# Optimization experiments

Measured on AMD Instinct MI355X. Metric: run time of the kernel, lower is better.

The kernel has to match this reference:

```python
import jax, jax.numpy as jnp
import numpy as np

B, S, D, H, DH = 2, 4096, 768, 12, 64
L = 2                      # encoder layers (reduced-depth longformer-base)
HW = 256                   # one-sided sliding window (attention_window = 512)
C = 2 * HW                 # query chunk size
NC = S // C                # number of chunks
KW = C + 2 * HW            # key-window length per chunk
V = 50265
SEP_ID, NSEP = 2, 32       # </s> token id; SEPs per block (fixed by construction)
G = NSEP + 1               # global tokens: <s> at pos 0 + all SEPs
NCLS = 5
EPS = 1e-5
NEG = -1e9


def layer_norm(x, gb):
    m = jnp.mean(x, -1, keepdims=True)
    v = jnp.var(x, -1, keepdims=True)
    return (x - m) * jax.lax.rsqrt(v + EPS) * gb[0] + gb[1]


def split_heads(x):  # [B,S,D] -> [B,H,S,DH]
    return x.reshape(B, S, H, DH).transpose(0, 2, 1, 3)


def window_gather(x):  # [B,H,S,DH] -> [B,H,NC,KW,DH] overlapping key windows
    xp = jnp.pad(x, ((0, 0), (0, 0), (HW, HW), (0, 0)))
    idx = (jnp.arange(NC) * C)[:, None] + jnp.arange(KW)[None, :]
    return xp[:, :, idx, :]


def longformer_attn(x, amask, gpos, wqkv, bqkv, wqkv_g, bqkv_g, wo, bo):
    q = split_heads(x @ wqkv[0] + bqkv[0]) / np.float32(np.sqrt(DH))
    k = split_heads(x @ wqkv[1] + bqkv[1])
    v = split_heads(x @ wqkv[2] + bqkv[2])

    # ----- local sliding-window scores (banded, chunked) -----
    kw = window_gather(k)
    vw = window_gather(v)
    qc = q.reshape(B, H, NC, C, DH)
    s_loc = jnp.einsum('bhncd,bhnkd->bhnck', qc, kw)  # [B,H,NC,C,KW]

    rel = jnp.arange(KW)[None, :] - jnp.arange(C)[:, None]          # [C,KW]
    band_ok = (rel >= 0) & (rel <= 2 * HW)
    key_pos = (jnp.arange(NC) * C)[:, None] + jnp.arange(KW)[None, :] - HW
    in_b = (key_pos >= 0) & (key_pos < S)                            # [NC,KW]
    amp = jnp.pad(amask, ((0, 0), (HW, HW)))
    idx = (jnp.arange(NC) * C)[:, None] + jnp.arange(KW)[None, :]
    am_w = amp[:, idx] > 0                                           # [B,NC,KW]
    mask = band_ok[None, None, None] & in_b[None, None, :, None, :] & am_w[:, None, :, None, :]
    s_loc = jnp.where(mask, s_loc, NEG).reshape(B, H, S, KW)

    # ----- scores of every query against the G global keys -----
    gidx = gpos[:, None, :, None]                                    # [B,1,G,1]
    kg = jnp.take_along_axis(k, gidx, axis=2)                        # [B,H,G,DH]
    vg = jnp.take_along_axis(v, gidx, axis=2)
    s_glob = jnp.einsum('bhsd,bhgd->bhsg', q, kg)                    # [B,H,S,G]

    probs = jax.nn.softmax(jnp.concatenate([s_glob, s_loc], -1), -1)
    pg, pl = probs[..., :G], probs[..., G:]
    ctx = jnp.einsum('bhsg,bhgd->bhsd', pg, vg)
    ctx = ctx + jnp.einsum('bhnck,bhnkd->bhncd', pl.reshape(B, H, NC, C, KW), vw).reshape(B, H, S, DH)

    # ----- global tokens attend to everything (separate projections) -----
    qg = split_heads(x @ wqkv_g[0] + bqkv_g[0]) / np.float32(np.sqrt(DH))
    kgf = split_heads(x @ wqkv_g[1] + bqkv_g[1])
    vgf = split_heads(x @ wqkv_g[2] + bqkv_g[2])
    qg = jnp.take_along_axis(qg, gidx, axis=2)                       # [B,H,G,DH]
    s_g = jnp.einsum('bhgd,bhsd->bhgs', qg, kgf)                     # [B,H,G,S]
    s_g = jnp.where(amask[:, None, None, :] > 0, s_g, NEG)
    og = jnp.einsum('bhgs,bhsd->bhgd', jax.nn.softmax(s_g, -1), vgf)

    ctx_m = ctx.transpose(0, 2, 1, 3).reshape(B, S, D)
    og_m = og.transpose(0, 2, 1, 3).reshape(B, G, D)
    ctx_m = ctx_m.at[jnp.arange(B)[:, None], gpos].set(og_m)         # replace global rows
    return ctx_m @ wo + bo


def setup_inputs() -> dict:
    key = jax.random.key(0)
    ks = jax.random.split(key, 12)
    ids = jax.random.randint(ks[0], (B, S), 5, V, dtype=jnp.int32)
    sep_positions = (jnp.arange(NSEP) + 1) * (S // NSEP) - 1         # SEP every 128 toks
    ids = ids.at[:, sep_positions].set(SEP_ID).at[:, 0].set(0)       # <s> at pos 0
    att = jnp.ones((B, S), jnp.int32)

    def nrm(k, shp):
        return jax.random.normal(k, shp, jnp.float32) * 0.02

    ln = jnp.stack([jnp.ones(D, jnp.float32), jnp.zeros(D, jnp.float32)])
    return dict(
        input_ids=ids, attention_mask=att,
        word_emb=nrm(ks[1], (V, D)), pos_emb=nrm(ks[2], (S + 2, D)),
        type_emb=nrm(ks[3], (D,)), emb_ln=ln,
        Wqkv=nrm(ks[4], (L, 3, D, D)), bqkv=jnp.zeros((L, 3, D), jnp.float32),
        Wqkv_g=nrm(ks[5], (L, 3, D, D)), bqkv_g=jnp.zeros((L, 3, D), jnp.float32),
        Wo=nrm(ks[6], (L, D, D)), bo=jnp.zeros((L, D), jnp.float32),
        ln1=jnp.broadcast_to(ln, (L, 2, D)),
        Wff1=nrm(ks[7], (L, D, 4 * D)), bff1=jnp.zeros((L, 4 * D), jnp.float32),
        Wff2=nrm(ks[8], (L, 4 * D, D)), bff2=jnp.zeros((L, D), jnp.float32),
        ln2=jnp.broadcast_to(ln, (L, 2, D)),
        cls_W=nrm(ks[9], (NCLS, D)), cls_b=jnp.zeros((NCLS,), jnp.float32),
    )


def reference(input_ids, attention_mask, word_emb, pos_emb, type_emb, emb_ln,
              Wqkv, bqkv, Wqkv_g, bqkv_g, Wo, bo, ln1, Wff1, bff1, Wff2, bff2,
              ln2, cls_W, cls_b):
    # global attention mask: pos 0 + every SEP (fixed count by construction)
    sep_pos = jnp.sort(jnp.where(input_ids == SEP_ID, jnp.arange(S)[None, :], S), -1)[:, :NSEP]
    sep_pos = sep_pos.astype(jnp.int32)
    gpos = jnp.concatenate([jnp.zeros((B, 1), jnp.int32), sep_pos], 1)  # [B,G]

    x = word_emb[input_ids] + pos_emb[jnp.arange(S) + 2][None] + type_emb
    x = layer_norm(x, emb_ln)
    for l in range(L):
        a = longformer_attn(x, attention_mask, gpos, Wqkv[l], bqkv[l],
                            Wqkv_g[l], bqkv_g[l], Wo[l], bo[l])
        x = layer_norm(x + a, ln1[l])
        f = jax.nn.gelu(x @ Wff1[l] + bff1[l], approximate=False) @ Wff2[l] + bff2[l]
        x = layer_norm(x + f, ln2[l])

    # gather SEP embeddings (row-major over batch then sentence) -> classifier
    h = jnp.take_along_axis(x, sep_pos[:, :, None], axis=1).reshape(B * NSEP, D)
    return h @ cls_W.T + cls_b
```

## Files before the change

### kernel.cpp

```cpp
#include <hip/hip_runtime.h>


#define Bb 2
#define Ss 4096
#define Dd 768
#define Hh 12
#define Gg 33
#define NSEPn 32
#define Ll 2
#define SPAD 4640
#define PADL 256
#define NCLSn 5
#define NCH 16
#define PARTF 1056
#define PSTR 72

typedef unsigned short u16;
typedef __attribute__((ext_vector_type(8))) short bv8;
typedef __attribute__((ext_vector_type(4))) short sv4;
typedef __attribute__((ext_vector_type(4))) float f32x4;

__device__ __forceinline__ float bf2f(u16 u) {
  unsigned v = ((unsigned)u) << 16;
  return __builtin_bit_cast(float, v);
}
__device__ __forceinline__ u16 f2bf(float f) {
  unsigned u = __builtin_bit_cast(unsigned, f);
  u += 0x7fffu + ((u >> 16) & 1u);
  return (u16)(u >> 16);
}
__device__ __forceinline__ void glds16(const void* g, void* l) {
  __builtin_amdgcn_global_load_lds(
      (const __attribute__((address_space(1))) void*)g,
      (__attribute__((address_space(3))) void*)l, 16, 0, 0);
}

__global__ void sep_find_kernel(const int* __restrict__ ids, int* __restrict__ cnt,
                                int* __restrict__ list) {
  int i = blockIdx.x * 256 + threadIdx.x;
  if (i >= Bb * Ss) return;
  int b = i >> 12;
  if (ids[i] == 2) {
    int idx = atomicAdd(&cnt[b], 1);
    if (idx < 64) list[b * 64 + idx] = i & (Ss - 1);
  }
}

__global__ void sep_sort_kernel(const int* __restrict__ cnt, const int* __restrict__ list,
                                int* __restrict__ gpos) {
  int b = blockIdx.x;
  int t = threadIdx.x;
  int n = cnt[b]; if (n > 64) n = 64;
  if (t < Gg) gpos[b * Gg + t] = (t == 0) ? 0 : (Ss - 1);
  __syncthreads();
  if (t < n) {
    int v = list[b * 64 + t];
    int rank = 0;
    for (int j = 0; j < n; ++j) rank += (list[b * 64 + j] < v) ? 1 : 0;
    if (rank < NSEPn) gpos[b * Gg + 1 + rank] = v;
  }
}

__global__ __launch_bounds__(256)
void wconv_kernel(const float* __restrict__ src0, u16* __restrict__ dst0,
                  int K, int N, int grp, long unit, long WLs) {
  __shared__ float t[32][33];
  int z = blockIdx.z;
  const float* src = src0 + (size_t)z * K * N;
  u16* dst = dst0 + (size_t)(z / grp) * WLs + (size_t)(z % grp) * unit;
  int n0 = blockIdx.x * 32, k0 = blockIdx.y * 32;
  int tx = threadIdx.x & 31, ty = threadIdx.x >> 5;
  #pragma unroll
  for (int i = 0; i < 4; ++i)
    t[ty + i * 8][tx] = src[(size_t)(k0 + ty + i * 8) * N + n0 + tx];
  __syncthreads();
  #pragma unroll
  for (int i = 0; i < 4; ++i)
    dst[(size_t)(n0 + ty + i * 8) * K + k0 + tx] = f2bf(t[tx][ty + i * 8]);
}

__global__ __launch_bounds__(256)
void embed_ln_kernel(const int* __restrict__ ids, const float* __restrict__ we,
                     const float* __restrict__ pe, const float* __restrict__ te,
                     const float* __restrict__ lnp, float* __restrict__ x,
                     u16* __restrict__ xb) {
  int row = blockIdx.x;
  int s = row & (Ss - 1);
  int id = ids[row];
  int tid = threadIdx.x;
  float v[3]; float sm = 0.f, s2 = 0.f;
  #pragma unroll
  for (int i = 0; i < 3; ++i) {
    int c = tid + i * 256;
    float t = we[(size_t)id * Dd + c] + pe[(size_t)(s + 2) * Dd + c] + te[c];
    v[i] = t; sm += t; s2 += t * t;
  }
  __shared__ float r1[256], r2[256];
  r1[tid] = sm; r2[tid] = s2; __syncthreads();
  for (int o = 128; o; o >>= 1) {
    if (tid < o) { r1[tid] += r1[tid + o]; r2[tid] += r2[tid + o]; }
    __syncthreads();
  }
  float mean = r1[0] * (1.f / 768.f);
  float var  = r2[0] * (1.f / 768.f) - mean * mean;
  float rs = rsqrtf(var + 1e-5f);
  #pragma unroll
  for (int i = 0; i < 3; ++i) {
    int c = tid + i * 256;
    float o = (v[i] - mean) * rs * lnp[c] + lnp[Dd + c];
    x[(size_t)row * Dd + c] = o;
    xb[(size_t)row * Dd + c] = f2bf(o);
  }
}

__global__ __launch_bounds__(256)
void add_ln3_kernel(const float* __restrict__ xin, const float* __restrict__ y0,
                    const float* __restrict__ y1, const float* __restrict__ lnp,
                    float* __restrict__ xout, u16* __restrict__ xbout) {
  int row = blockIdx.x;
  int tid = threadIdx.x;
  float v[3]; float sm = 0.f, s2 = 0.f;
  #pragma unroll
  for (int i = 0; i < 3; ++i) {
    int c = tid + i * 256;
    size_t idx = (size_t)row * Dd + c;
    float t = xin[idx] + y0[idx] + y1[idx];
    v[i] = t; sm += t; s2 += t * t;
  }
  __shared__ float r1[256], r2[256];
  r1[tid] = sm; r2[tid] = s2; __syncthreads();
  for (int o = 128; o; o >>= 1) {
    if (tid < o) { r1[tid] += r1[tid + o]; r2[tid] += r2[tid + o]; }
    __syncthreads();
  }
  float mean = r1[0] * (1.f / 768.f);
  float var  = r2[0] * (1.f / 768.f) - mean * mean;
  float rs = rsqrtf(var + 1e-5f);
  #pragma unroll
  for (int i = 0; i < 3; ++i) {
    int c = tid + i * 256;
    float o = (v[i] - mean) * rs * lnp[c] + lnp[Dd + c];
    xout[(size_t)row * Dd + c] = o;
    xbout[(size_t)row * Dd + c] = f2bf(o);
  }
}

template <int MODE>
__global__ __launch_bounds__(256)
void gemm2_kernel(const u16* __restrict__ A, const u16* __restrict__ Bt,
                  const float* __restrict__ bias, float* __restrict__ outf,
                  float* __restrict__ outf2,
                  u16* __restrict__ o0, u16* __restrict__ o1, u16* __restrict__ o2,
                  int N, int Ks, int Kl, float scale) {
  __shared__ u16 la[2][128 * 32], lb[2][128 * 32];
  int tid = threadIdx.x;
  int wave = tid >> 6, lane = tid & 63;
  int wr = wave >> 1, wc = wave & 1;
  int lg = lane >> 4, lc = lane & 15;
  int row0 = blockIdx.y * 128, col0 = blockIdx.x * 128;
  int koff = blockIdx.z * Kl;

  const u16* Ag = A + (size_t)(row0 + wave * 32 + (lane >> 2)) * Ks + (lane & 3) * 8 + koff;
  const u16* Bg = Bt + (size_t)(col0 + wave * 32 + (lane >> 2)) * Ks + (lane & 3) * 8 + koff;
  int wofs = wave * 1024;

  f32x4 acc[4][4];
  #pragma unroll
  for (int m = 0; m < 4; ++m)
    #pragma unroll
    for (int n = 0; n < 4; ++n) acc[m][n] = (f32x4){0.f, 0.f, 0.f, 0.f};

  glds16(Ag, la[0] + wofs);
  glds16(Ag + (size_t)16 * Ks, la[0] + wofs + 512);
  glds16(Bg, lb[0] + wofs);
  glds16(Bg + (size_t)16 * Ks, lb[0] + wofs + 512);
  __syncthreads();

  int nk = Kl >> 5;
  for (int t = 0; t < nk; ++t) {
    int cur = t & 1;
    if (t + 1 < nk) {
      int k1 = (t + 1) << 5;
      glds16(Ag + k1, la[cur ^ 1] + wofs);
      glds16(Ag + (size_t)16 * Ks + k1, la[cur ^ 1] + wofs + 512);
      glds16(Bg + k1, lb[cur ^ 1] + wofs);
      glds16(Bg + (size_t)16 * Ks + k1, lb[cur ^ 1] + wofs + 512);
    }
    bv8 af[4], bf_[4];
    #pragma unroll
    for (int m = 0; m < 4; ++m)
      af[m] = *reinterpret_cast<const bv8*>(la[cur] + (wr * 64 + m * 16 + lc) * 32 + lg * 8);
    #pragma unroll
    for (int n = 0; n < 4; ++n)
      bf_[n] = *reinterpret_cast<const bv8*>(lb[cur] + (wc * 64 + n * 16 + lc) * 32 + lg * 8);
    __builtin_amdgcn_s_setprio(1);
    #pragma unroll
    for (int m = 0; m < 4; ++m)
      #pragma unroll
      for (int n = 0; n < 4; ++n)
        acc[m][n] = __builtin_amdgcn_mfma_f32_16x16x32_bf16(af[m], bf_[n], acc[m][n], 0, 0, 0);
    __builtin_amdgcn_s_setprio(0);
    __syncthreads();
  }

  #pragma unroll
  for (int m = 0; m < 4; ++m) {
    int grow0 = row0 + wr * 64 + m * 16 + lg * 4;
    #pragma unroll
    for (int n = 0; n < 4; ++n) {
      int gcol = col0 + wc * 64 + n * 16 + lc;
      float bvl = bias[gcol];
      if (MODE == 0) {
        float* od = blockIdx.z ? outf2 : outf;
        float badd = blockIdx.z ? 0.f : bvl;
        #pragma unroll
        for (int r = 0; r < 4; ++r)
          od[(size_t)(grow0 + r) * N + gcol] = acc[m][n][r] + badd;
      } else if (MODE == 1) {
        #pragma unroll
        for (int r = 0; r < 4; ++r) {
          float v = acc[m][n][r] + bvl;
          v = 0.5f * v * (1.0f + erff(v * 0.70710678118654752f));
          o0[(size_t)(grow0 + r) * N + gcol] = f2bf(v);
        }
      } else if (MODE == 4) {
        #pragma unroll
        for (int r = 0; r < 4; ++r)
          o0[(size_t)(grow0 + r) * N + gcol] = f2bf((acc[m][n][r] + bvl) * scale);
      } else if (MODE == 2) {
        int sec = col0 >= 1536 ? 2 : (col0 >= 768 ? 1 : 0);
        int colr = gcol - sec * 768;
        int hh = colr >> 6, d = colr & 63;
        int bb = grow0 >> 12, s = grow0 & (Ss - 1);
        size_t bhh = (size_t)(bb * Hh + hh);
        if (sec == 0) {
          #pragma unroll
          for (int r = 0; r < 4; ++r)
            o0[(bhh * Ss + s + r) * 64 + d] = f2bf((acc[m][n][r] + bvl) * scale);
        } else if (sec == 1) {
          #pragma unroll
          for (int r = 0; r < 4; ++r)
            o1[(bhh * SPAD + PADL + s + r) * 64 + d] = f2bf(acc[m][n][r] + bvl);
        } else {
          sv4 pk;
          #pragma unroll
          for (int r = 0; r < 4; ++r) pk[r] = (short)f2bf(acc[m][n][r] + bvl);
          *reinterpret_cast<sv4*>(o2 + (bhh * 64 + d) * SPAD + PADL + s) = pk;
        }
      } else if (MODE == 3) {
        int sec = col0 >= 768 ? 1 : 0;
        int colr = gcol - sec * 768;
        int hh = colr >> 6, d = colr & 63;
        int bb = grow0 >> 12, s = grow0 & (Ss - 1);
        size_t bhh = (size_t)(bb * Hh + hh);
        if (sec == 0) {
          #pragma unroll
          for (int r = 0; r < 4; ++r)
            o0[(bhh * Ss + s + r) * 64 + d] = f2bf(acc[m][n][r] + bvl);
        } else {
          sv4 pk;
          #pragma unroll
          for (int r = 0; r < 4; ++r) pk[r] = (short)f2bf(acc[m][n][r] + bvl);
          *reinterpret_cast<sv4*>(o1 + (bhh * 64 + d) * Ss + s) = pk;
        }
      }
    }
  }
}

__global__ __launch_bounds__(256)
void gather_glob_kernel(const u16* __restrict__ kpk, const u16* __restrict__ vtpk,
                        const int* __restrict__ gpos, u16* __restrict__ kg,
                        u16* __restrict__ vgt) {
  int bh = blockIdx.x;
  int b = bh / Hh;
  int tid = threadIdx.x;
  for (int idx = tid; idx < 64 * 64; idx += 256) {
    int g = idx >> 6, d = idx & 63;
    u16 kv = 0, vv = 0;
    if (g < Gg) {
      int p = gpos[b * Gg + g];
      kv = kpk[((size_t)bh * SPAD + PADL + p) * 64 + d];
      vv = vtpk[((size_t)bh * 64 + d) * SPAD + PADL + p];
    }
    kg[(size_t)bh * 4096 + idx] = kv;
    vgt[((size_t)bh * 64 + d) * 64 + g] = vv;
  }
}

__global__ __launch_bounds__(256)
void gather_xg_kernel(const u16* __restrict__ xb, const int* __restrict__ gpos,
                      u16* __restrict__ xg) {
  int rg = blockIdx.x;
  int b = rg / Gg;
  int p = gpos[rg];
  int tid = threadIdx.x;
  for (int c = tid; c < Dd; c += 256)
    xg[(size_t)rg * Dd + c] = xb[((size_t)b * Ss + p) * Dd + c];
}

#define LOCAL_NB (Bb * Hh * (Ss / 64))
__global__ __launch_bounds__(256)
void attn_local_kernel(const u16* __restrict__ qpk, const u16* __restrict__ kpk,
                       const u16* __restrict__ vtpk, const u16* __restrict__ kg,
                       const u16* __restrict__ vgt, const int* __restrict__ amask,
                       u16* __restrict__ ctx) {
  __shared__ u16 Plds[4][16 * PSTR];
  int bid = blockIdx.x;
  int swz = (bid & 7) * (LOCAL_NB / 8) + (bid >> 3);
  int qb = swz & 63;
  int bh = swz >> 6;
  int b = bh / Hh;
  int h = bh - b * Hh;
  int wv = threadIdx.x >> 6;
  int q0 = qb * 64 + wv * 16;
  int lane = threadIdx.x & 63;
  int lg = lane >> 4, lc = lane & 15;
  int lg4 = lg * 4;
  int q = q0 + lc;

  const u16* qbase = qpk + (((size_t)bh) * Ss + q0) * 64;
  bv8 aq0 = *reinterpret_cast<const bv8*>(qbase + (size_t)lc * 64 + lg * 8);
  bv8 aq1 = *reinterpret_cast<const bv8*>(qbase + (size_t)lc * 64 + 32 + lg * 8);

  f32x4 o[4];
  #pragma unroll
  for (int i = 0; i < 4; ++i) o[i] = (f32x4){0.f, 0.f, 0.f, 0.f};
  float mrun = -1e30f, lrun = 0.f;

  const u16* kgb = kg + ((size_t)bh) * 64 * 64;
  const u16* vgb = vgt + ((size_t)bh) * 64 * 64;
  const u16* kb = kpk + ((size_t)bh) * SPAD * 64;
  const u16* vb = vtpk + ((size_t)bh) * 64 * SPAD;
  const int* amb = amask + b * Ss;
  u16* P = &Plds[wv][0];

  bv8 kc[8];
  #pragma unroll
  for (int j = 0; j < 4; ++j) {
    const u16* kr = kgb + (size_t)(j * 16 + lc) * 64;
    kc[2 * j]     = *reinterpret_cast<const bv8*>(kr + lg * 8);
    kc[2 * j + 1] = *reinterpret_cast<const bv8*>(kr + 32 + lg * 8);
  }
  int amvN;
  { int ni = min(max(q0 - 256 + lane, 0), Ss - 1); amvN = amb[ni]; }

  for (int step = 0; step < 10; ++step) {
    bool isg = (step == 0);
    int ks = isg ? 0 : (q0 - 256 + (step - 1) * 64);
    int amvC = amvN;
    if (step < 9) { int ni = min(max(q0 - 256 + step * 64 + lane, 0), Ss - 1); amvN = amb[ni]; }

    bv8 vf[8];
    #pragma unroll
    for (int j2 = 0; j2 < 2; ++j2)
      #pragma unroll
      for (int nt = 0; nt < 4; ++nt) {
        const u16* vr = isg ? (vgb + (size_t)(nt * 16 + lc) * 64 + j2 * 32)
                            : (vb + (size_t)(nt * 16 + lc) * SPAD + PADL + ks + j2 * 32);
        vf[j2 * 4 + nt] = *reinterpret_cast<const bv8*>(vr + lg * 8);
      }
    bv8 kn[8];
    if (step < 9) {
      int ksn = q0 - 256 + step * 64;
      #pragma unroll
      for (int j = 0; j < 4; ++j) {
        const u16* kr = kb + (size_t)(PADL + ksn + j * 16 + lc) * 64;
        kn[2 * j]     = *reinterpret_cast<const bv8*>(kr + lg * 8);
        kn[2 * j + 1] = *reinterpret_cast<const bv8*>(kr + 32 + lg * 8);
      }
    }
    unsigned long long kmask;
    if (isg) {
      kmask = (1ull << Gg) - 1;
    } else {
      int kidx = ks + lane;
      kmask = __ballot((kidx >= 0) && (kidx < Ss) && (amvC > 0));
    }
    f32x4 sc[4];
    __builtin_amdgcn_s_setprio(1);
    #pragma unroll
    for (int j = 0; j < 4; ++j) {
      f32x4 z = (f32x4){0.f, 0.f, 0.f, 0.f};
      sc[j] = __builtin_amdgcn_mfma_f32_16x16x32_bf16(kc[2 * j], aq0, z, 0, 0, 0);
      sc[j] = __builtin_amdgcn_mfma_f32_16x16x32_bf16(kc[2 * j + 1], aq1, sc[j], 0, 0, 0);
    }
    __builtin_amdgcn_s_setprio(0);
    float mloc = -1e30f;
    bool fast = (!isg) && (step >= 2) && (step <= 8) && (kmask == ~0ull);
    if (fast) {
      #pragma unroll
      for (int j = 0; j < 4; ++j)
        #pragma unroll
        for (int r = 0; r < 4; ++r) mloc = fmaxf(mloc, sc[j][r]);
    } else {
      #pragma unroll
      for (int j = 0; j < 4; ++j)
        #pragma unroll
        for (int r = 0; r < 4; ++r) {
          int kk = ks + j * 16 + lg4 + r;
          bool ok = (kmask >> (j * 16 + lg4 + r)) & 1;
          if (!isg) ok = ok && ((unsigned)(kk - q + 256) <= 512u);
          sc[j][r] = ok ? sc[j][r] : -1e9f;
          mloc = fmaxf(mloc, sc[j][r]);
        }
    }
    mloc = fmaxf(mloc, __shfl_xor(mloc, 16));
    mloc = fmaxf(mloc, __shfl_xor(mloc, 32));
    if (__any(mloc > mrun)) {
      float nm = fmaxf(mrun, mloc);
      float scal = __expf(mrun - nm);
      mrun = nm;
      lrun *= scal;
      #pragma unroll
      for (int r = 0; r < 4; ++r) {
        float sr = __shfl(scal, lg4 + r);
        #pragma unroll
        for (int nt = 0; nt < 4; ++nt) o[nt][r] *= sr;
      }
    }
    float psum = 0.f;
    #pragma unroll
    for (int j = 0; j < 4; ++j) {
      sv4 pk;
      #pragma unroll
      for (int r = 0; r < 4; ++r) {
        float p = __expf(sc[j][r] - mrun);
        psum += p;
        pk[r] = (short)f2bf(p);
      }
      *reinterpret_cast<sv4*>(P + lc * PSTR + j * 16 + lg4) = pk;
    }
    psum += __shfl_xor(psum, 16);
    psum += __shfl_xor(psum, 32);
    lrun += psum;
    __builtin_amdgcn_s_setprio(1);
    #pragma unroll
    for (int j2 = 0; j2 < 2; ++j2) {
      bv8 ap = *reinterpret_cast<const bv8*>(P + lc * PSTR + j2 * 32 + lg * 8);
      #pragma unroll
      for (int nt = 0; nt < 4; ++nt)
        o[nt] = __builtin_amdgcn_mfma_f32_16x16x32_bf16(ap, vf[j2 * 4 + nt], o[nt], 0, 0, 0);
    }
    __builtin_amdgcn_s_setprio(0);
    if (step < 9) {
      #pragma unroll
      for (int i = 0; i < 8; ++i) kc[i] = kn[i];
    }
  }
  float inv = 1.0f / lrun;
  #pragma unroll
  for (int r = 0; r < 4; ++r) {
    float invr = __shfl(inv, lg4 + r);
    size_t rowoff = ((size_t)b * Ss + q0 + lg4 + r) * Dd + h * 64;
    #pragma unroll
    for (int nt = 0; nt < 4; ++nt)
      ctx[rowoff + nt * 16 + lc] = f2bf(o[nt][r] * invr);
  }
}

__global__ __launch_bounds__(192)
void attn_globalq_kernel(const u16* __restrict__ qgb, const u16* __restrict__ kgf,
                         const u16* __restrict__ vgt, const int* __restrict__ amask,
                         float* __restrict__ part) {
  __shared__ u16 Plds[3][16 * 32];
  int blk = blockIdx.x;
  int ch = blk & (NCH - 1);
  int bh = blk / NCH;
  int b = bh / Hh, h = bh - b * Hh;
  int wv = threadIdx.x >> 6;
  int lane = threadIdx.x & 63;
  int lg = lane >> 4, lc = lane & 15;

  int qrow = wv * 16 + lc;
  bv8 aq0 = (bv8)0, aq1 = (bv8)0;
  if (qrow < Gg) {
    const u16* qr = qgb + (size_t)(b * Gg + qrow) * Dd + h * 64;
    aq0 = *reinterpret_cast<const bv8*>(qr + lg * 8);
    aq1 = *reinterpret_cast<const bv8*>(qr + 32 + lg * 8);
  }

  f32x4 o[4];
  float mrun[4], lrun[4];
  #pragma unroll
  for (int i = 0; i < 4; ++i) { o[i] = (f32x4){0.f,0.f,0.f,0.f}; mrun[i] = -1e30f; lrun[i] = 0.f; }

  const u16* kb = kgf + ((size_t)bh) * Ss * 64;
  const u16* vb = vgt + ((size_t)bh) * 64 * Ss;
  const int* amb = amask + b * Ss;
  int ks0 = ch * (Ss / NCH);

  for (int st = 0; st < (Ss / NCH) / 32; ++st) {
    int ks = ks0 + st * 32;
    f32x4 sc0, sc1;
    {
      const u16* kr0 = kb + (size_t)(ks + lc) * 64;
      const u16* kr1 = kr0 + 16 * 64;
      bv8 b00 = *reinterpret_cast<const bv8*>(kr0 + lg * 8);
      bv8 b01 = *reinterpret_cast<const bv8*>(kr0 + 32 + lg * 8);
      bv8 b10 = *reinterpret_cast<const bv8*>(kr1 + lg * 8);
      bv8 b11 = *reinterpret_cast<const bv8*>(kr1 + 32 + lg * 8);
      f32x4 z = (f32x4){0.f,0.f,0.f,0.f};
      sc0 = __builtin_amdgcn_mfma_f32_16x16x32_bf16(aq0, b00, z, 0, 0, 0);
      sc0 = __builtin_amdgcn_mfma_f32_16x16x32_bf16(aq1, b01, sc0, 0, 0, 0);
      sc1 = __builtin_amdgcn_mfma_f32_16x16x32_bf16(aq0, b10, z, 0, 0, 0);
      sc1 = __builtin_amdgcn_mfma_f32_16x16x32_bf16(aq1, b11, sc1, 0, 0, 0);
    }
    bool v0 = amb[ks + lc] > 0;
    bool v1 = amb[ks + 16 + lc] > 0;
    #pragma unroll
    for (int r = 0; r < 4; ++r) {
      float s0 = v0 ? sc0[r] : -1e9f;
      float s1 = v1 ? sc1[r] : -1e9f;
      float rm = fmaxf(s0, s1);
      #pragma unroll
      for (int off = 1; off < 16; off <<= 1) rm = fmaxf(rm, __shfl_xor(rm, off));
      float nm = fmaxf(mrun[r], rm);
      float scal = __expf(mrun[r] - nm);
      float p0 = __expf(s0 - nm);
      float p1 = __expf(s1 - nm);
      float ps = p0 + p1;
      #pragma unroll
      for (int off = 1; off < 16; off <<= 1) ps += __shfl_xor(ps, off);
      lrun[r] = lrun[r] * scal + ps;
      mrun[r] = nm;
      #pragma unroll
      for (int nt = 0; nt < 4; ++nt) o[nt][r] *= scal;
      int prow = lg * 4 + r;
      Plds[wv][prow * 32 + lc] = f2bf(p0);
      Plds[wv][prow * 32 + 16 + lc] = f2bf(p1);
    }
    bv8 ap = *reinterpret_cast<const bv8*>(&Plds[wv][lc * 32 + lg * 8]);
    #pragma unroll
    for (int nt = 0; nt < 4; ++nt) {
      const u16* vr = vb + (size_t)(nt * 16 + lc) * Ss + ks;
      bv8 bvv = *reinterpret_cast<const bv8*>(vr + lg * 8);
      o[nt] = __builtin_amdgcn_mfma_f32_16x16x32_bf16(ap, bvv, o[nt], 0, 0, 0);
    }
  }

  float* pb = part + ((size_t)(bh * 3 + wv) * NCH + ch) * PARTF;
  #pragma unroll
  for (int r = 0; r < 4; ++r) {
    int row = lg * 4 + r;
    #pragma unroll
    for (int nt = 0; nt < 4; ++nt)
      pb[row * 64 + nt * 16 + lc] = o[nt][r];
    if (lc == 0) {
      pb[1024 + row] = mrun[r];
      pb[1040 + row] = lrun[r];
    }
  }
}

__global__ __launch_bounds__(256)
void attn_gmerge_kernel(const float* __restrict__ part, const int* __restrict__ gpos,
                        u16* __restrict__ ctx) {
  __shared__ float wgt[Gg][NCH];
  __shared__ float sinvl[Gg];
  int bh = blockIdx.x;
  int b = bh / Hh, h = bh - b * Hh;
  int tid = threadIdx.x;
  if (tid < Gg) {
    int qt = tid >> 4, rr = tid & 15;
    const float* pb = part + ((size_t)(bh * 3 + qt) * NCH) * PARTF;
    float mx = -1e30f;
    for (int c = 0; c < NCH; ++c) mx = fmaxf(mx, pb[c * PARTF + 1024 + rr]);
    float l = 0.f;
    for (int c = 0; c < NCH; ++c) {
      float w = __expf(pb[c * PARTF + 1024 + rr] - mx);
      wgt[tid][c] = w;
      l += w * pb[c * PARTF + 1040 + rr];
    }
    sinvl[tid] = 1.0f / l;
  }
  __syncthreads();
  for (int e = tid; e < Gg * 64; e += 256) {
    int row = e >> 6, d = e & 63;
    int qt = row >> 4, rr = row & 15;
    const float* pb = part + ((size_t)(bh * 3 + qt) * NCH) * PARTF + rr * 64 + d;
    float acc = 0.f;
    #pragma unroll
    for (int c = 0; c < NCH; ++c) acc += wgt[row][c] * pb[c * PARTF];
    int pos = gpos[b * Gg + row];
    ctx[((size_t)b * Ss + pos) * Dd + h * 64 + d] = f2bf(acc * sinvl[row]);
  }
}

__global__ __launch_bounds__(64)
void cls_kernel(const float* __restrict__ x, const float* __restrict__ W,
                const float* __restrict__ bias, const int* __restrict__ gpos,
                float* __restrict__ out) {
  int r = blockIdx.x;
  int b = r >> 5, i = r & 31;
  int pos = gpos[b * Gg + 1 + i];
  int lane = threadIdx.x;
  const float* xr = x + ((size_t)b * Ss + pos) * Dd;
  float acc[NCLSn] = {0.f, 0.f, 0.f, 0.f, 0.f};
  for (int k = lane; k < Dd; k += 64) {
    float xv = xr[k];
    #pragma unroll
    for (int c = 0; c < NCLSn; ++c) acc[c] += xv * W[c * Dd + k];
  }
  #pragma unroll
  for (int c = 0; c < NCLSn; ++c) {
    #pragma unroll
    for (int off = 1; off < 64; off <<= 1) acc[c] += __shfl_xor(acc[c], off);
  }
  if (lane == 0) {
    #pragma unroll
    for (int c = 0; c < NCLSn; ++c) out[r * NCLSn + c] = acc[c] + bias[c];
  }
}

extern "C" void kernel_launch(void* const* d_in, const int* in_sizes, int n_in,
                              void* d_out, int out_size, void* d_ws, size_t ws_size,
                              hipStream_t stream) {
  const int* ids     = (const int*)d_in[0];
  const int* amask   = (const int*)d_in[1];
  const float* we    = (const float*)d_in[2];
  const float* pe    = (const float*)d_in[3];
  const float* te    = (const float*)d_in[4];
  const float* embln = (const float*)d_in[5];
  const float* Wqkv  = (const float*)d_in[6];
  const float* bqkv  = (const float*)d_in[7];
  const float* Wqkvg = (const float*)d_in[8];
  const float* bqkvg = (const float*)d_in[9];
  const float* Wo    = (const float*)d_in[10];
  const float* bo    = (const float*)d_in[11];
  const float* ln1   = (const float*)d_in[12];
  const float* Wff1  = (const float*)d_in[13];
  const float* bff1  = (const float*)d_in[14];
  const float* Wff2  = (const float*)d_in[15];
  const float* bff2  = (const float*)d_in[16];
  const float* ln2   = (const float*)d_in[17];
  const float* clsW  = (const float*)d_in[18];
  const float* clsb  = (const float*)d_in[19];
  float* out = (float*)d_out;

  char* ws = (char*)d_ws;
  size_t off = 0;
  auto alloc = [&](size_t bytes) { size_t o = off; off += (bytes + 255) & ~(size_t)255; return o; };

  const size_t DD = (size_t)Dd * Dd;
  const size_t DF = (size_t)Dd * 4 * Dd;
  const size_t WL = 7 * DD + 2 * DF;

  size_t o_cnt  = alloc(Bb * 4);
  size_t o_list = alloc(Bb * 64 * 4);
  size_t o_gpos = alloc(Bb * Gg * 4);
  size_t o_w    = alloc(WL * Ll * 2);
  size_t o_x    = alloc((size_t)Bb * Ss * Dd * 4);
  size_t o_xb   = alloc((size_t)Bb * Ss * Dd * 2);
  size_t o_kgf  = alloc((size_t)Bb * Hh * Ss * 64 * 2);
  size_t o_vgf  = alloc((size_t)Bb * Hh * Ss * 64 * 2);
  size_t o_accB = o_kgf;
  size_t o_qpk  = alloc((size_t)Bb * Hh * Ss * 64 * 2);
  size_t o_kpk  = alloc((size_t)Bb * Hh * SPAD * 64 * 2);
  size_t o_vtpk = alloc((size_t)Bb * Hh * 64 * SPAD * 2);
  size_t o_kg   = alloc((size_t)Bb * Hh * 64 * 64 * 2);
  size_t o_vgt  = alloc((size_t)Bb * Hh * 64 * 64 * 2);
  size_t o_xg   = alloc((size_t)128 * Dd * 2);
  size_t o_qg   = alloc((size_t)128 * Dd * 2);
  size_t o_part = alloc((size_t)Bb * Hh * 3 * NCH * PARTF * 4);
  size_t o_f1b  = o_qpk;
  {
    size_t f1b_bytes = (size_t)Bb * Ss * 4 * Dd * 2;
    if (off - o_qpk < f1b_bytes) off = o_qpk + ((f1b_bytes + 255) & ~(size_t)255);
  }
  size_t o_ctx = alloc((size_t)Bb * Ss * Dd * 2);
  size_t o_acc = alloc((size_t)Bb * Ss * Dd * 4);
  if (ws_size < off) return;

  u16* Wb = (u16*)(ws + o_w);
  int* gposp = (int*)(ws + o_gpos);
  float* accA = (float*)(ws + o_acc);
  float* accB = (float*)(ws + o_accB);

  (void)hipMemsetAsync(ws + o_cnt, 0, Bb * 4, stream);
  (void)hipMemsetAsync(ws + o_kpk, 0, (size_t)Bb * Hh * SPAD * 64 * 2, stream);
  (void)hipMemsetAsync(ws + o_vtpk, 0, (size_t)Bb * Hh * 64 * SPAD * 2, stream);
  (void)hipMemsetAsync(ws + o_xg, 0, (size_t)128 * Dd * 2, stream);

  sep_find_kernel<<<(Bb * Ss + 255) / 256, 256, 0, stream>>>(ids, (int*)(ws + o_cnt), (int*)(ws + o_list));
  sep_sort_kernel<<<Bb, 64, 0, stream>>>((int*)(ws + o_cnt), (int*)(ws + o_list), gposp);

  wconv_kernel<<<dim3(24, 24, 6), 256, 0, stream>>>(Wqkv,  Wb,          Dd, Dd, 3, (long)DD, (long)WL);
  wconv_kernel<<<dim3(24, 24, 6), 256, 0, stream>>>(Wqkvg, Wb + 3 * DD, Dd, Dd, 3, (long)DD, (long)WL);
  wconv_kernel<<<dim3(24, 24, 2), 256, 0, stream>>>(Wo,    Wb + 6 * DD, Dd, Dd, 1, 0L, (long)WL);
  wconv_kernel<<<dim3(96, 24, 2), 256, 0, stream>>>(Wff1,  Wb + 7 * DD, Dd, 4 * Dd, 1, 0L, (long)WL);
  wconv_kernel<<<dim3(24, 96, 2), 256, 0, stream>>>(Wff2,  Wb + 7 * DD + DF, 4 * Dd, Dd, 1, 0L, (long)WL);

  embed_ln_kernel<<<Bb * Ss, 256, 0, stream>>>(ids, we, pe, te, embln, (float*)(ws + o_x), (u16*)(ws + o_xb));

  for (int l = 0; l < Ll; ++l) {
    size_t wb = (size_t)l * WL;
    u16* xb = (u16*)(ws + o_xb);
    gemm2_kernel<2><<<dim3(18, 64), 256, 0, stream>>>(xb, Wb + wb, bqkv + (size_t)l * 3 * Dd, nullptr, nullptr,
        (u16*)(ws + o_qpk), (u16*)(ws + o_kpk), (u16*)(ws + o_vtpk), 2304, Dd, Dd, 0.125f);
    gather_glob_kernel<<<Bb * Hh, 256, 0, stream>>>((u16*)(ws + o_kpk), (u16*)(ws + o_vtpk), gposp, (u16*)(ws + o_kg), (u16*)(ws + o_vgt));
    gather_xg_kernel<<<Bb * Gg, 256, 0, stream>>>(xb, gposp, (u16*)(ws + o_xg));
    gemm2_kernel<4><<<dim3(6, 1), 256, 0, stream>>>((u16*)(ws + o_xg), Wb + wb + 3 * DD, bqkvg + (size_t)l * 3 * Dd, nullptr, nullptr,
        (u16*)(ws + o_qg), nullptr, nullptr, Dd, Dd, Dd, 0.125f);
    gemm2_kernel<3><<<dim3(12, 64), 256, 0, stream>>>(xb, Wb + wb + 4 * DD, bqkvg + (size_t)(l * 3 + 1) * Dd, nullptr, nullptr,
        (u16*)(ws + o_kgf), (u16*)(ws + o_vgf), nullptr, 1536, Dd, Dd, 1.0f);
    attn_local_kernel<<<LOCAL_NB, 256, 0, stream>>>((u16*)(ws + o_qpk), (u16*)(ws + o_kpk), (u16*)(ws + o_vtpk), (u16*)(ws + o_kg), (u16*)(ws + o_vgt), amask, (u16*)(ws + o_ctx));
    attn_globalq_kernel<<<Bb * Hh * NCH, 192, 0, stream>>>((u16*)(ws + o_qg), (u16*)(ws + o_kgf), (u16*)(ws + o_vgf), amask, (float*)(ws + o_part));
    attn_gmerge_kernel<<<Bb * Hh, 256, 0, stream>>>((float*)(ws + o_part), gposp, (u16*)(ws + o_ctx));
    gemm2_kernel<0><<<dim3(6, 64, 2), 256, 0, stream>>>((u16*)(ws + o_ctx), Wb + wb + 6 * DD, bo + (size_t)l * Dd, accA, accB,
        nullptr, nullptr, nullptr, Dd, Dd, Dd / 2, 1.0f);
    add_ln3_kernel<<<Bb * Ss, 256, 0, stream>>>((float*)(ws + o_x), accA, accB, ln1 + (size_t)l * 2 * Dd, (float*)(ws + o_x), xb);
    gemm2_kernel<1><<<dim3(24, 64), 256, 0, stream>>>(xb, Wb + wb + 7 * DD, bff1 + (size_t)l * 4 * Dd, nullptr, nullptr,
        (u16*)(ws + o_f1b), nullptr, nullptr, 4 * Dd, Dd, Dd, 1.0f);
    gemm2_kernel<0><<<dim3(6, 64, 2), 256, 0, stream>>>((u16*)(ws + o_f1b), Wb + wb + 7 * DD + DF, bff2 + (size_t)l * Dd, accA, accB,
        nullptr, nullptr, nullptr, Dd, 4 * Dd, 2 * Dd, 1.0f);
    add_ln3_kernel<<<Bb * Ss, 256, 0, stream>>>((float*)(ws + o_x), accA, accB, ln2 + (size_t)l * 2 * Dd, (float*)(ws + o_x), xb);
  }

  cls_kernel<<<Bb * NSEPn, 64, 0, stream>>>((float*)(ws + o_x), clsW, clsb, gposp, out);
}
```

Measured before the change: 889.1 us.

## Fuse local QKV and global K/V projections into one GEMM; drop K double buffer

The weight layout is rearranged so the local QKV weights and the global K and V weights sit side by side, with the global Q weights moved to the end. This lets a single 3840-column GEMM write Q, K, V and the global K/V outputs, replacing two launches over the same activations. The biases are packed into a contiguous workspace buffer with device copies to match. In the local attention kernel, the next K tile is now loaded straight into the current K registers after the score MFMAs, instead of into a separate prefetch buffer, which frees registers but gives the load less time to overlap.

Result: no change. 875.7 us (-1.5%).

```diff
diff --git a/kernel.cpp b/kernel.cpp
--- a/kernel.cpp
+++ b/kernel.cpp
@@ -63,10 +63,10 @@
 
 __global__ __launch_bounds__(256)
 void wconv_kernel(const float* __restrict__ src0, u16* __restrict__ dst0,
-                  int K, int N, int grp, long unit, long WLs) {
+                  int K, int N, int grp, int sstr, long unit, long WLs) {
   __shared__ float t[32][33];
   int z = blockIdx.z;
-  const float* src = src0 + (size_t)z * K * N;
+  const float* src = src0 + (size_t)((z / grp) * sstr + (z % grp)) * K * N;
   u16* dst = dst0 + (size_t)(z / grp) * WLs + (size_t)(z % grp) * unit;
   int n0 = blockIdx.x * 32, k0 = blockIdx.y * 32;
   int tx = threadIdx.x & 31, ty = threadIdx.x >> 5;
@@ -151,6 +151,7 @@
                   const float* __restrict__ bias, float* __restrict__ outf,
                   float* __restrict__ outf2,
                   u16* __restrict__ o0, u16* __restrict__ o1, u16* __restrict__ o2,
+                  u16* __restrict__ o3, u16* __restrict__ o4,
                   int N, int Ks, int Kl, float scale) {
   __shared__ u16 la[2][128 * 32], lb[2][128 * 32];
   int tid = threadIdx.x;
@@ -228,7 +229,7 @@
         for (int r = 0; r < 4; ++r)
           o0[(size_t)(grow0 + r) * N + gcol] = f2bf((acc[m][n][r] + bvl) * scale);
       } else if (MODE == 2) {
-        int sec = col0 >= 1536 ? 2 : (col0 >= 768 ? 1 : 0);
+        int sec = (col0 >> 7) / 6;
         int colr = gcol - sec * 768;
         int hh = colr >> 6, d = colr & 63;
         int bb = grow0 >> 12, s = grow0 & (Ss - 1);
@@ -241,27 +242,20 @@
           #pragma unroll
           for (int r = 0; r < 4; ++r)
             o1[(bhh * SPAD + PADL + s + r) * 64 + d] = f2bf(acc[m][n][r] + bvl);
+        } else if (sec == 2) {
+          sv4 pk;
+          #pragma unroll
+          for (int r = 0; r < 4; ++r) pk[r] = (short)f2bf(acc[m][n][r] + bvl);
+          *reinterpret_cast<sv4*>(o2 + (bhh * 64 + d) * SPAD + PADL + s) = pk;
+        } else if (sec == 3) {
+          #pragma unroll
+          for (int r = 0; r < 4; ++r)
+            o3[(bhh * Ss + s + r) * 64 + d] = f2bf(acc[m][n][r] + bvl);
         } else {
           sv4 pk;
           #pragma unroll
           for (int r = 0; r < 4; ++r) pk[r] = (short)f2bf(acc[m][n][r] + bvl);
-          *reinterpret_cast<sv4*>(o2 + (bhh * 64 + d) * SPAD + PADL + s) = pk;
-        }
-      } else if (MODE == 3) {
-        int sec = col0 >= 768 ? 1 : 0;
-        int colr = gcol - sec * 768;
-        int hh = colr >> 6, d = colr & 63;
-        int bb = grow0 >> 12, s = grow0 & (Ss - 1);
-        size_t bhh = (size_t)(bb * Hh + hh);
-        if (sec == 0) {
-          #pragma unroll
-          for (int r = 0; r < 4; ++r)
-            o0[(bhh * Ss + s + r) * 64 + d] = f2bf(acc[m][n][r] + bvl);
-        } else {
-          sv4 pk;
-          #pragma unroll
-          for (int r = 0; r < 4; ++r) pk[r] = (short)f2bf(acc[m][n][r] + bvl);
-          *reinterpret_cast<sv4*>(o1 + (bhh * 64 + d) * Ss + s) = pk;
+          *reinterpret_cast<sv4*>(o4 + (bhh * 64 + d) * Ss + s) = pk;
         }
       }
     }
@@ -360,16 +354,6 @@
                             : (vb + (size_t)(nt * 16 + lc) * SPAD + PADL + ks + j2 * 32);
         vf[j2 * 4 + nt] = *reinterpret_cast<const bv8*>(vr + lg * 8);
       }
-    bv8 kn[8];
-    if (step < 9) {
-      int ksn = q0 - 256 + step * 64;
-      #pragma unroll
-      for (int j = 0; j < 4; ++j) {
-        const u16* kr = kb + (size_t)(PADL + ksn + j * 16 + lc) * 64;
-        kn[2 * j]     = *reinterpret_cast<const bv8*>(kr + lg * 8);
-        kn[2 * j + 1] = *reinterpret_cast<const bv8*>(kr + 32 + lg * 8);
-      }
-    }
     unsigned long long kmask;
     if (isg) {
       kmask = (1ull << Gg) - 1;
@@ -386,6 +370,15 @@
       sc[j] = __builtin_amdgcn_mfma_f32_16x16x32_bf16(kc[2 * j + 1], aq1, sc[j], 0, 0, 0);
     }
     __builtin_amdgcn_s_setprio(0);
+    if (step < 9) {
+      int ksn = q0 - 256 + step * 64;
+      #pragma unroll
+      for (int j = 0; j < 4; ++j) {
+        const u16* kr = kb + (size_t)(PADL + ksn + j * 16 + lc) * 64;
+        kc[2 * j]     = *reinterpret_cast<const bv8*>(kr + lg * 8);
+        kc[2 * j + 1] = *reinterpret_cast<const bv8*>(kr + 32 + lg * 8);
+      }
+    }
     float mloc = -1e30f;
     bool fast = (!isg) && (step >= 2) && (step <= 8) && (kmask == ~0ull);
     if (fast) {
@@ -443,10 +436,6 @@
         o[nt] = __builtin_amdgcn_mfma_f32_16x16x32_bf16(ap, vf[j2 * 4 + nt], o[nt], 0, 0, 0);
     }
     __builtin_amdgcn_s_setprio(0);
-    if (step < 9) {
-      #pragma unroll
-      for (int i = 0; i < 8; ++i) kc[i] = kn[i];
-    }
   }
   float inv = 1.0f / lrun;
   #pragma unroll
@@ -649,6 +638,7 @@
   size_t o_cnt  = alloc(Bb * 4);
   size_t o_list = alloc(Bb * 64 * 4);
   size_t o_gpos = alloc(Bb * Gg * 4);
+  size_t o_bias = alloc((size_t)Ll * 3840 * 4);
   size_t o_w    = alloc(WL * Ll * 2);
   size_t o_x    = alloc((size_t)Bb * Ss * Dd * 4);
   size_t o_xb   = alloc((size_t)Bb * Ss * Dd * 2);
@@ -682,38 +672,48 @@
   (void)hipMemsetAsync(ws + o_vtpk, 0, (size_t)Bb * Hh * 64 * SPAD * 2, stream);
   (void)hipMemsetAsync(ws + o_xg, 0, (size_t)128 * Dd * 2, stream);
 
+  for (int l = 0; l < Ll; ++l) {
+    (void)hipMemcpyAsync(ws + o_bias + (size_t)l * 3840 * 4, bqkv + (size_t)l * 3 * Dd,
+                         3 * Dd * 4, hipMemcpyDeviceToDevice, stream);
+    (void)hipMemcpyAsync(ws + o_bias + (size_t)l * 3840 * 4 + 3 * Dd * 4,
+                         bqkvg + (size_t)(l * 3 + 1) * Dd,
+                         2 * Dd * 4, hipMemcpyDeviceToDevice, stream);
+  }
+
   sep_find_kernel<<<(Bb * Ss + 255) / 256, 256, 0, stream>>>(ids, (int*)(ws + o_cnt), (int*)(ws + o_list));
   sep_sort_kernel<<<Bb, 64, 0, stream>>>((int*)(ws + o_cnt), (int*)(ws + o_list), gposp);
 
-  wconv_kernel<<<dim3(24, 24, 6), 256, 0, stream>>>(Wqkv,  Wb,          Dd, Dd, 3, (long)DD, (long)WL);
-  wconv_kernel<<<dim3(24, 24, 6), 256, 0, stream>>>(Wqkvg, Wb + 3 * DD, Dd, Dd, 3, (long)DD, (long)WL);
-  wconv_kernel<<<dim3(24, 24, 2), 256, 0, stream>>>(Wo,    Wb + 6 * DD, Dd, Dd, 1, 0L, (long)WL);
-  wconv_kernel<<<dim3(96, 24, 2), 256, 0, stream>>>(Wff1,  Wb + 7 * DD, Dd, 4 * Dd, 1, 0L, (long)WL);
-  wconv_kernel<<<dim3(24, 96, 2), 256, 0, stream>>>(Wff2,  Wb + 7 * DD + DF, 4 * Dd, Dd, 1, 0L, (long)WL);
+  wconv_kernel<<<dim3(24, 24, 6), 256, 0, stream>>>(Wqkv,       Wb,          Dd, Dd, 3, 3, (long)DD, (long)WL);
+  wconv_kernel<<<dim3(24, 24, 2), 256, 0, stream>>>(Wqkvg + DD,     Wb + 3 * DD, Dd, Dd, 1, 3, 0L, (long)WL);
+  wconv_kernel<<<dim3(24, 24, 2), 256, 0, stream>>>(Wqkvg + 2 * DD, Wb + 4 * DD, Dd, Dd, 1, 3, 0L, (long)WL);
+  wconv_kernel<<<dim3(24, 24, 2), 256, 0, stream>>>(Wqkvg,          Wb + 5 * DD, Dd, Dd, 1, 3, 0L, (long)WL);
+  wconv_kernel<<<dim3(24, 24, 2), 256, 0, stream>>>(Wo,         Wb + 6 * DD, Dd, Dd, 1, 1, 0L, (long)WL);
+  wconv_kernel<<<dim3(96, 24, 2), 256, 0, stream>>>(Wff1,       Wb + 7 * DD, Dd, 4 * Dd, 1, 1, 0L, (long)WL);
+  wconv_kernel<<<dim3(24, 96, 2), 256, 0, stream>>>(Wff2,       Wb + 7 * DD + DF, 4 * Dd, Dd, 1, 1, 0L, (long)WL);
 
   embed_ln_kernel<<<Bb * Ss, 256, 0, stream>>>(ids, we, pe, te, embln, (float*)(ws + o_x), (u16*)(ws + o_xb));
 
   for (int l = 0; l < Ll; ++l) {
     size_t wb = (size_t)l * WL;
     u16* xb = (u16*)(ws + o_xb);
-    gemm2_kernel<2><<<dim3(18, 64), 256, 0, stream>>>(xb, Wb + wb, bqkv + (size_t)l * 3 * Dd, nullptr, nullptr,
-        (u16*)(ws + o_qpk), (u16*)(ws + o_kpk), (u16*)(ws + o_vtpk), 2304, Dd, Dd, 0.125f);
+    gemm2_kernel<2><<<dim3(30, 64), 256, 0, stream>>>(xb, Wb + wb, (float*)(ws + o_bias) + (size_t)l * 3840,
+        nullptr, nullptr,
+        (u16*)(ws + o_qpk), (u16*)(ws + o_kpk), (u16*)(ws + o_vtpk),
+        (u16*)(ws + o_kgf), (u16*)(ws + o_vgf), 3840, Dd, Dd, 0.125f);
     gather_glob_kernel<<<Bb * Hh, 256, 0, stream>>>((u16*)(ws + o_kpk), (u16*)(ws + o_vtpk), gposp, (u16*)(ws + o_kg), (u16*)(ws + o_vgt));
     gather_xg_kernel<<<Bb * Gg, 256, 0, stream>>>(xb, gposp, (u16*)(ws + o_xg));
-    gemm2_kernel<4><<<dim3(6, 1), 256, 0, stream>>>((u16*)(ws + o_xg), Wb + wb + 3 * DD, bqkvg + (size_t)l * 3 * Dd, nullptr, nullptr,
-        (u16*)(ws + o_qg), nullptr, nullptr, Dd, Dd, Dd, 0.125f);
-    gemm2_kernel<3><<<dim3(12, 64), 256, 0, stream>>>(xb, Wb + wb + 4 * DD, bqkvg + (size_t)(l * 3 + 1) * Dd, nullptr, nullptr,
-        (u16*)(ws + o_kgf), (u16*)(ws + o_vgf), nullptr, 1536, Dd, Dd, 1.0f);
+    gemm2_kernel<4><<<dim3(6, 1), 256, 0, stream>>>((u16*)(ws + o_xg), Wb + wb + 5 * DD, bqkvg + (size_t)l * 3 * Dd,
+        nullptr, nullptr, (u16*)(ws + o_qg), nullptr, nullptr, nullptr, nullptr, Dd, Dd, Dd, 0.125f);
     attn_local_kernel<<<LOCAL_NB, 256, 0, stream>>>((u16*)(ws + o_qpk), (u16*)(ws + o_kpk), (u16*)(ws + o_vtpk), (u16*)(ws + o_kg), (u16*)(ws + o_vgt), amask, (u16*)(ws + o_ctx));
     attn_globalq_kernel<<<Bb * Hh * NCH, 192, 0, stream>>>((u16*)(ws + o_qg), (u16*)(ws + o_kgf), (u16*)(ws + o_vgf), amask, (float*)(ws + o_part));
     attn_gmerge_kernel<<<Bb * Hh, 256, 0, stream>>>((float*)(ws + o_part), gposp, (u16*)(ws + o_ctx));
     gemm2_kernel<0><<<dim3(6, 64, 2), 256, 0, stream>>>((u16*)(ws + o_ctx), Wb + wb + 6 * DD, bo + (size_t)l * Dd, accA, accB,
-        nullptr, nullptr, nullptr, Dd, Dd, Dd / 2, 1.0f);
+        nullptr, nullptr, nullptr, nullptr, nullptr, Dd, Dd, Dd / 2, 1.0f);
     add_ln3_kernel<<<Bb * Ss, 256, 0, stream>>>((float*)(ws + o_x), accA, accB, ln1 + (size_t)l * 2 * Dd, (float*)(ws + o_x), xb);
     gemm2_kernel<1><<<dim3(24, 64), 256, 0, stream>>>(xb, Wb + wb + 7 * DD, bff1 + (size_t)l * 4 * Dd, nullptr, nullptr,
-        (u16*)(ws + o_f1b), nullptr, nullptr, 4 * Dd, Dd, Dd, 1.0f);
+        (u16*)(ws + o_f1b), nullptr, nullptr, nullptr, nullptr, 4 * Dd, Dd, Dd, 1.0f);
     gemm2_kernel<0><<<dim3(6, 64, 2), 256, 0, stream>>>((u16*)(ws + o_f1b), Wb + wb + 7 * DD + DF, bff2 + (size_t)l * Dd, accA, accB,
-        nullptr, nullptr, nullptr, Dd, 4 * Dd, 2 * Dd, 1.0f);
+        nullptr, nullptr, nullptr, nullptr, nullptr, Dd, 4 * Dd, 2 * Dd, 1.0f);
     add_ln3_kernel<<<Bb * Ss, 256, 0, stream>>>((float*)(ws + o_x), accA, accB, ln2 + (size_t)l * 2 * Dd, (float*)(ws + o_x), xb);
   }
 
```
